# Optimization experiments

Hardware: AMD Instinct MI355X
Metric: run time of the kernel (lower is better)

The kernel has to match this reference:

```python
import jax, jax.numpy as jnp
import numpy as np

H = 4  # hidden size fixed by the module


def setup_inputs() -> dict:
    key = jax.random.key(0)
    ks = jax.random.split(key, 7)
    B, T, I = 4096, 1024, 8
    s_ih = 1.0 / np.sqrt(H)
    return {
        "x": jax.random.normal(ks[0], (B, T, I), dtype=jnp.float32),
        "W_ih": jax.random.uniform(ks[1], (4 * H, I), jnp.float32, -s_ih, s_ih),
        "W_hh": jax.random.uniform(ks[2], (4 * H, H), jnp.float32, -s_ih, s_ih),
        "b_ih": jax.random.uniform(ks[3], (4 * H,), jnp.float32, -s_ih, s_ih),
        "b_hh": jax.random.uniform(ks[4], (4 * H,), jnp.float32, -s_ih, s_ih),
        "fc_w": jax.random.uniform(ks[5], (1, H), jnp.float32, -0.5, 0.5),
        "fc_b": jax.random.uniform(ks[6], (1,), jnp.float32, -0.5, 0.5),
    }


def _lstm_last_hidden(x, W_ih, W_hh, b_ih, b_hh):
    B = x.shape[0]
    # Precompute input contribution for all timesteps: [B, T, 4H] -> scan over T
    xg = jnp.einsum("bti,gi->btg", x, W_ih) + (b_ih + b_hh)
    xg = jnp.swapaxes(xg, 0, 1)  # [T, B, 4H]

    def step(carry, g_t):
        h, c = carry
        gates = g_t + h @ W_hh.T  # [B, 4H]
        i, f, g, o = jnp.split(gates, 4, axis=-1)  # PyTorch gate order
        c = jax.nn.sigmoid(f) * c + jax.nn.sigmoid(i) * jnp.tanh(g)
        h = jax.nn.sigmoid(o) * jnp.tanh(c)
        return (h, c), None

    h0 = jnp.zeros((B, H), dtype=x.dtype)
    (h_last, _), _ = jax.lax.scan(step, (h0, h0), xg)
    return h_last  # [B, H]


def reference(x, W_ih, W_hh, b_ih, b_hh, fc_w, fc_b):
    h_last = _lstm_last_hidden(x, W_ih, W_hh, b_ih, b_hh)
    return h_last @ fc_w.T + fc_b  # [B, 1]
```

## Files before the change

kernel.cpp:

```cpp
#include <hip/hip_runtime.h>


#define TT 1024
#define II 8
#define CHUNK 32
#define NCHUNK (TT / CHUNK)
#define ROW (CHUNK * II)
#define SPAD 4

typedef float v2f __attribute__((ext_vector_type(2)));

template <int CTRL>
__device__ __forceinline__ float dppf(float v) {
  return __int_as_float(
      __builtin_amdgcn_mov_dpp(__float_as_int(v), CTRL, 0xF, 0xF, true));
}

__device__ __forceinline__ float fast_sigmoid(float x) {
  return __builtin_amdgcn_rcpf(1.0f + __expf(-x));
}

__device__ __forceinline__ float fast_tanh(float x) {
  return 1.0f - 2.0f * __builtin_amdgcn_rcpf(__expf(2.0f * x) + 1.0f);
}

#define GLOAD_LDS16(gp, lp)                                   \
  __builtin_amdgcn_global_load_lds(                           \
      (const __attribute__((address_space(1))) void*)(gp),    \
      (__attribute__((address_space(3))) void*)(lp), 16, 0, 0)

__global__ __launch_bounds__(64, 1) void lstm_fused(
    const float* __restrict__ x, const float* __restrict__ W_ih,
    const float* __restrict__ W_hh, const float* __restrict__ b_ih,
    const float* __restrict__ b_hh, const float* __restrict__ fc_w,
    const float* __restrict__ fc_b, float* __restrict__ out, int B) {
  const int lane = threadIdx.x;
  const int j = lane & 3;
  const int grp = lane >> 2;
  const int b = blockIdx.x * 16 + grp;

  __shared__ float xs0[16][ROW + SPAD];
  __shared__ float xs1[16][ROW + SPAD];

  v2f wih01[II], wih23[II], whh01[4], whh23[4];
  v2f bias01, bias23;
#pragma unroll
  for (int k = 0; k < II; ++k) {
    wih01[k] = v2f{W_ih[(0 * 4 + j) * II + k], W_ih[(1 * 4 + j) * II + k]};
    wih23[k] = v2f{W_ih[(2 * 4 + j) * II + k], W_ih[(3 * 4 + j) * II + k]};
  }
#pragma unroll
  for (int k = 0; k < 4; ++k) {
    whh01[k] = v2f{W_hh[(0 * 4 + j) * 4 + k], W_hh[(1 * 4 + j) * 4 + k]};
    whh23[k] = v2f{W_hh[(2 * 4 + j) * 4 + k], W_hh[(3 * 4 + j) * 4 + k]};
  }
  bias01 = v2f{b_ih[0 * 4 + j] + b_hh[0 * 4 + j],
               b_ih[1 * 4 + j] + b_hh[1 * 4 + j]};
  bias23 = v2f{b_ih[2 * 4 + j] + b_hh[2 * 4 + j],
               b_ih[3 * 4 + j] + b_hh[3 * 4 + j]};

  const size_t blockBase = (size_t)blockIdx.x * 16;

  auto issue0 = [&](int t0) {
#pragma unroll
    for (int s = 0; s < 16; ++s) {
      const float* gp = x + (blockBase + s) * (TT * II) + t0 * II + lane * 4;
      GLOAD_LDS16(gp, &xs0[s][0]);
    }
  };
  auto issue1 = [&](int t0) {
#pragma unroll
    for (int s = 0; s < 16; ++s) {
      const float* gp = x + (blockBase + s) * (TT * II) + t0 * II + lane * 4;
      GLOAD_LDS16(gp, &xs1[s][0]);
    }
  };

  float h = 0.0f, c = 0.0f;

  auto step = [&](float4 xa, float4 xb) {
    v2f a01 = bias01, a23 = bias23;
#define XFMA(k, val)                                      \
  {                                                       \
    v2f xv = v2f{(val), (val)};                           \
    a01 = __builtin_elementwise_fma(wih01[k], xv, a01);   \
    a23 = __builtin_elementwise_fma(wih23[k], xv, a23);   \
  }
    XFMA(0, xa.x) XFMA(1, xa.y) XFMA(2, xa.z) XFMA(3, xa.w)
    XFMA(4, xb.x) XFMA(5, xb.y) XFMA(6, xb.z) XFMA(7, xb.w)
#undef XFMA
    const float h0 = dppf<0x00>(h);
    const float h1 = dppf<0x55>(h);
    const float h2 = dppf<0xAA>(h);
    const float h3 = dppf<0xFF>(h);
#define HFMA(k, val)                                      \
  {                                                       \
    v2f hv = v2f{(val), (val)};                           \
    a01 = __builtin_elementwise_fma(whh01[k], hv, a01);   \
    a23 = __builtin_elementwise_fma(whh23[k], hv, a23);   \
  }
    HFMA(0, h0) HFMA(1, h1) HFMA(2, h2) HFMA(3, h3)
#undef HFMA
    const float ig = fast_sigmoid(a01.x);
    const float fg = fast_sigmoid(a01.y);
    const float gg = fast_tanh(a23.x);
    const float og = fast_sigmoid(a23.y);
    c = fmaf(fg, c, ig * gg);
    h = og * fast_tanh(c);
  };

  auto compute_chunk = [&](const float (*xs)[ROW + SPAD]) {
    const float* row = &xs[grp][0];
    float4 xa = *(const float4*)(row);
    float4 xb = *(const float4*)(row + 4);
#pragma unroll 4
    for (int u = 0; u < CHUNK; ++u) {
      const int un = (u + 1 < CHUNK) ? (u + 1) : u;
      const float4 na = *(const float4*)(row + un * 8);
      const float4 nb = *(const float4*)(row + un * 8 + 4);
      step(xa, xb);
      xa = na;
      xb = nb;
    }
  };

  issue0(0);
  issue1(CHUNK);

  for (int ck = 0; ck < NCHUNK; ck += 2) {
    compute_chunk(xs0);
    if (ck + 2 < NCHUNK) issue0((ck + 2) * CHUNK);
    compute_chunk(xs1);
    if (ck + 3 < NCHUNK) issue1((ck + 3) * CHUNK);
  }

  float v = h * fc_w[j];
  v += dppf<0xB1>(v);
  v += dppf<0x4E>(v);
  if (j == 0 && b < B) out[b] = v + fc_b[0];
}

extern "C" void kernel_launch(void* const* d_in, const int* in_sizes, int n_in,
                              void* d_out, int out_size, void* d_ws,
                              size_t ws_size, hipStream_t stream) {
  const float* x = (const float*)d_in[0];
  const float* W_ih = (const float*)d_in[1];
  const float* W_hh = (const float*)d_in[2];
  const float* b_ih = (const float*)d_in[3];
  const float* b_hh = (const float*)d_in[4];
  const float* fc_w = (const float*)d_in[5];
  const float* fc_b = (const float*)d_in[6];
  float* out = (float*)d_out;

  const int B = in_sizes[0] / (TT * II);
  const int nblocks = (B + 15) / 16;
  lstm_fused<<<nblocks, 64, 0, stream>>>(x, W_ih, W_hh, b_ih, b_hh, fc_w, fc_b,
                                         out, B);
}
```

Before: 316.8 us.

## Split LSTM into producer wave for input projection and consumer wave for recurrence

Each block now has two waves. A producer wave loads x chunks into LDS and computes the input-gate projections (W_ih·x plus bias) into double-buffered LDS tiles. A consumer wave reads those precomputed gates and runs only the serial recurrent update. This takes the input FMAs out of the latency-bound recurrence loop so they can run in parallel on another SIMD. The cost is extra LDS traffic, a second LDS buffer set, and a block-wide barrier every chunk.

```diff
diff --git a/kernel.cpp b/kernel.cpp
--- a/kernel.cpp
+++ b/kernel.cpp
@@ -29,115 +29,129 @@
       (const __attribute__((address_space(1))) void*)(gp),    \
       (__attribute__((address_space(3))) void*)(lp), 16, 0, 0)
 
-__global__ __launch_bounds__(64, 1) void lstm_fused(
+__global__ __launch_bounds__(128, 1) void lstm_fused(
     const float* __restrict__ x, const float* __restrict__ W_ih,
     const float* __restrict__ W_hh, const float* __restrict__ b_ih,
     const float* __restrict__ b_hh, const float* __restrict__ fc_w,
     const float* __restrict__ fc_b, float* __restrict__ out, int B) {
-  const int lane = threadIdx.x;
+  const int tid = threadIdx.x;
+  const int wave = tid >> 6;
+  const int lane = tid & 63;
   const int j = lane & 3;
   const int grp = lane >> 2;
   const int b = blockIdx.x * 16 + grp;
 
   __shared__ float xs0[16][ROW + SPAD];
   __shared__ float xs1[16][ROW + SPAD];
+  __shared__ float pa0[CHUNK][16][16];
+  __shared__ float pa1[CHUNK][16][16];
 
-  v2f wih01[II], wih23[II], whh01[4], whh23[4];
-  v2f bias01, bias23;
+  if (wave == 0) {
+    v2f wih01[II], wih23[II];
+    v2f bias01, bias23;
 #pragma unroll
-  for (int k = 0; k < II; ++k) {
-    wih01[k] = v2f{W_ih[(0 * 4 + j) * II + k], W_ih[(1 * 4 + j) * II + k]};
-    wih23[k] = v2f{W_ih[(2 * 4 + j) * II + k], W_ih[(3 * 4 + j) * II + k]};
+    for (int k = 0; k < II; ++k) {
+      wih01[k] = v2f{W_ih[(0 * 4 + j) * II + k], W_ih[(1 * 4 + j) * II + k]};
+      wih23[k] = v2f{W_ih[(2 * 4 + j) * II + k], W_ih[(3 * 4 + j) * II + k]};
+    }
+    bias01 = v2f{b_ih[0 * 4 + j] + b_hh[0 * 4 + j],
+                 b_ih[1 * 4 + j] + b_hh[1 * 4 + j]};
+    bias23 = v2f{b_ih[2 * 4 + j] + b_hh[2 * 4 + j],
+                 b_ih[3 * 4 + j] + b_hh[3 * 4 + j]};
+
+    const size_t blockBase = (size_t)blockIdx.x * 16;
+
+    auto issue = [&](float(*xs)[ROW + SPAD], int t0) {
+#pragma unroll
+      for (int s = 0; s < 16; ++s) {
+        const float* gp =
+            x + (blockBase + s) * (TT * II) + (size_t)t0 * II + lane * 4;
+        GLOAD_LDS16(gp, &xs[s][0]);
+      }
+    };
+
+    auto produce = [&](float(*pa)[16][16], const float(*xs)[ROW + SPAD]) {
+      const float* row = &xs[grp][0];
+#pragma unroll 8
+      for (int u = 0; u < CHUNK; ++u) {
+        const float4 xa = *(const float4*)(row + u * 8);
+        const float4 xb = *(const float4*)(row + u * 8 + 4);
+        v2f a01 = bias01, a23 = bias23;
+#define XFMA(k, val)                                    \
+  {                                                     \
+    v2f xv = v2f{(val), (val)};                         \
+    a01 = __builtin_elementwise_fma(wih01[k], xv, a01); \
+    a23 = __builtin_elementwise_fma(wih23[k], xv, a23); \
   }
+        XFMA(0, xa.x) XFMA(1, xa.y) XFMA(2, xa.z) XFMA(3, xa.w)
+        XFMA(4, xb.x) XFMA(5, xb.y) XFMA(6, xb.z) XFMA(7, xb.w)
+#undef XFMA
+        *(float4*)&pa[u][grp][j * 4] = float4{a01.x, a01.y, a23.x, a23.y};
+      }
+    };
+
+    issue(xs0, 0);
+    issue(xs1, CHUNK);
+    produce(pa0, xs0);
+    __syncthreads();
+
+    for (int ck = 0; ck < NCHUNK; ++ck) {
+      if (ck + 1 < NCHUNK)
+        produce(((ck + 1) & 1) ? pa1 : pa0, ((ck + 1) & 1) ? xs1 : xs0);
+      if (ck + 2 < NCHUNK) issue((ck & 1) ? xs1 : xs0, (ck + 2) * CHUNK);
+      __syncthreads();
+    }
+  } else {
+    v2f whh01[4], whh23[4];
 #pragma unroll
-  for (int k = 0; k < 4; ++k) {
-    whh01[k] = v2f{W_hh[(0 * 4 + j) * 4 + k], W_hh[(1 * 4 + j) * 4 + k]};
-    whh23[k] = v2f{W_hh[(2 * 4 + j) * 4 + k], W_hh[(3 * 4 + j) * 4 + k]};
+    for (int k = 0; k < 4; ++k) {
+      whh01[k] = v2f{W_hh[(0 * 4 + j) * 4 + k], W_hh[(1 * 4 + j) * 4 + k]};
+      whh23[k] = v2f{W_hh[(2 * 4 + j) * 4 + k], W_hh[(3 * 4 + j) * 4 + k]};
+    }
+    float h = 0.0f, c = 0.0f;
+
+    __syncthreads();
+
+    for (int ck = 0; ck < NCHUNK; ++ck) {
+      const float(*pa)[16][16] = (ck & 1) ? pa1 : pa0;
+      const float* base = &pa[0][grp][j * 4];
+      float4 g = *(const float4*)base;
+#pragma unroll 8
+      for (int u = 0; u < CHUNK; ++u) {
+        const int un = (u + 1 < CHUNK) ? (u + 1) : u;
+        const float4 gn = *(const float4*)(base + un * 256);
+
+        v2f a01 = v2f{g.x, g.y};
+        v2f a23 = v2f{g.z, g.w};
+        const float h0 = dppf<0x00>(h);
+        const float h1 = dppf<0x55>(h);
+        const float h2 = dppf<0xAA>(h);
+        const float h3 = dppf<0xFF>(h);
+#define HFMA(k, val)                                    \
+  {                                                     \
+    v2f hv = v2f{(val), (val)};                         \
+    a01 = __builtin_elementwise_fma(whh01[k], hv, a01); \
+    a23 = __builtin_elementwise_fma(whh23[k], hv, a23); \
   }
-  bias01 = v2f{b_ih[0 * 4 + j] + b_hh[0 * 4 + j],
-               b_ih[1 * 4 + j] + b_hh[1 * 4 + j]};
-  bias23 = v2f{b_ih[2 * 4 + j] + b_hh[2 * 4 + j],
-               b_ih[3 * 4 + j] + b_hh[3 * 4 + j]};
+        HFMA(0, h0) HFMA(1, h1) HFMA(2, h2) HFMA(3, h3)
+#undef HFMA
+        const float ig = fast_sigmoid(a01.x);
+        const float fg = fast_sigmoid(a01.y);
+        const float gg = fast_tanh(a23.x);
+        const float og = fast_sigmoid(a23.y);
+        c = fmaf(fg, c, ig * gg);
+        h = og * fast_tanh(c);
 
-  const size_t blockBase = (size_t)blockIdx.x * 16;
+        g = gn;
+      }
+      __syncthreads();
+    }
 
-  auto issue0 = [&](int t0) {
-#pragma unroll
-    for (int s = 0; s < 16; ++s) {
-      const float* gp = x + (blockBase + s) * (TT * II) + t0 * II + lane * 4;
-      GLOAD_LDS16(gp, &xs0[s][0]);
-    }
-  };
-  auto issue1 = [&](int t0) {
-#pragma unroll
-    for (int s = 0; s < 16; ++s) {
-      const float* gp = x + (blockBase + s) * (TT * II) + t0 * II + lane * 4;
-      GLOAD_LDS16(gp, &xs1[s][0]);
-    }
-  };
-
-  float h = 0.0f, c = 0.0f;
-
-  auto step = [&](float4 xa, float4 xb) {
-    v2f a01 = bias01, a23 = bias23;
-#define XFMA(k, val)                                      \
-  {                                                       \
-    v2f xv = v2f{(val), (val)};                           \
-    a01 = __builtin_elementwise_fma(wih01[k], xv, a01);   \
-    a23 = __builtin_elementwise_fma(wih23[k], xv, a23);   \
+    float v = h * fc_w[j];
+    v += dppf<0xB1>(v);
+    v += dppf<0x4E>(v);
+    if (j == 0 && b < B) out[b] = v + fc_b[0];
   }
-    XFMA(0, xa.x) XFMA(1, xa.y) XFMA(2, xa.z) XFMA(3, xa.w)
-    XFMA(4, xb.x) XFMA(5, xb.y) XFMA(6, xb.z) XFMA(7, xb.w)
-#undef XFMA
-    const float h0 = dppf<0x00>(h);
-    const float h1 = dppf<0x55>(h);
-    const float h2 = dppf<0xAA>(h);
-    const float h3 = dppf<0xFF>(h);
-#define HFMA(k, val)                                      \
-  {                                                       \
-    v2f hv = v2f{(val), (val)};                           \
-    a01 = __builtin_elementwise_fma(whh01[k], hv, a01);   \
-    a23 = __builtin_elementwise_fma(whh23[k], hv, a23);   \
-  }
-    HFMA(0, h0) HFMA(1, h1) HFMA(2, h2) HFMA(3, h3)
-#undef HFMA
-    const float ig = fast_sigmoid(a01.x);
-    const float fg = fast_sigmoid(a01.y);
-    const float gg = fast_tanh(a23.x);
-    const float og = fast_sigmoid(a23.y);
-    c = fmaf(fg, c, ig * gg);
-    h = og * fast_tanh(c);
-  };
-
-  auto compute_chunk = [&](const float (*xs)[ROW + SPAD]) {
-    const float* row = &xs[grp][0];
-    float4 xa = *(const float4*)(row);
-    float4 xb = *(const float4*)(row + 4);
-#pragma unroll 4
-    for (int u = 0; u < CHUNK; ++u) {
-      const int un = (u + 1 < CHUNK) ? (u + 1) : u;
-      const float4 na = *(const float4*)(row + un * 8);
-      const float4 nb = *(const float4*)(row + un * 8 + 4);
-      step(xa, xb);
-      xa = na;
-      xb = nb;
-    }
-  };
-
-  issue0(0);
-  issue1(CHUNK);
-
-  for (int ck = 0; ck < NCHUNK; ck += 2) {
-    compute_chunk(xs0);
-    if (ck + 2 < NCHUNK) issue0((ck + 2) * CHUNK);
-    compute_chunk(xs1);
-    if (ck + 3 < NCHUNK) issue1((ck + 3) * CHUNK);
-  }
-
-  float v = h * fc_w[j];
-  v += dppf<0xB1>(v);
-  v += dppf<0x4E>(v);
-  if (j == 0 && b < B) out[b] = v + fc_b[0];
 }
 
 extern "C" void kernel_launch(void* const* d_in, const int* in_sizes, int n_in,
@@ -154,6 +168,6 @@
 
   const int B = in_sizes[0] / (TT * II);
   const int nblocks = (B + 15) / 16;
-  lstm_fused<<<nblocks, 64, 0, stream>>>(x, W_ih, W_hh, b_ih, b_hh, fc_w, fc_b,
-                                         out, B);
+  lstm_fused<<<nblocks, 128, 0, stream>>>(x, W_ih, W_hh, b_ih, b_hh, fc_w,
+                                          fc_b, out, B);
 }
```

Result: faster. 260.1 us (-17.9%).
